# Optimization experiments

Hardware: AMD Instinct MI355X
Metric: run time of the kernel (lower is better)

Reference implementation:

```python
import jax, jax.numpy as jnp
import numpy as np

EPS = 1e-6       # eps from __init__
STEPSIZE = 1.0   # stepsize from __init__
DELTA = 0.1      # delta from __init__


def setup_inputs() -> dict:
    key = jax.random.key(0)
    k1, k2, k3 = jax.random.split(key, 3)
    N, L, H, E, M = 2, 2048, 8, 64, 64
    return {
        "queries": jax.random.normal(k1, (N, L, H, E), dtype=jnp.float32),
        "keys": jax.random.normal(k2, (N, L, H, E), dtype=jnp.float32),
        "values": jax.random.normal(k3, (N, L, H, M), dtype=jnp.float32),
        "key_lengths_mask": jnp.ones((N, L), dtype=jnp.float32),
    }


def reference(queries, keys, values, key_lengths_mask):
    # elu feature map: elu(x) + 1
    Q = jax.nn.elu(queries) + 1.0                                   # [N,L,H,E]
    K = (jax.nn.elu(keys) + 1.0) * key_lengths_mask[:, :, None, None]
    N, L, H, E = Q.shape

    # normalizer Z_t = 1 / (q_t . sum_{s<=t} k_s + eps)
    Z = 1.0 / (jnp.einsum('nlhe,nlhe->nlh', Q, jnp.cumsum(K, axis=1)) + EPS)

    # per-step outer products k_s v_s^T  (original materializes this einsum)
    KV = jnp.einsum('nlhe,nlhm->nlhem', K, values)                  # [N,L,H,E,M]

    # causal_dot_product: out_t = q_t . cumsum_s(KV)_t
    out = jnp.einsum('nlhe,nlhem->nlhm', Q, jnp.cumsum(KV, axis=1)) * Z[..., None]

    # momentum coefficients mu_j from Frobenius norms over (E,M)
    diff_norm = jnp.sqrt(jnp.sum((KV[:, 1:] - KV[:, :-1]) ** 2, axis=(3, 4)))  # [N,L-1,H]
    base_norm = jnp.sqrt(jnp.sum(KV[:, :-1] ** 2, axis=(3, 4)))
    mu = jnp.clip((1.0 - jnp.sqrt(diff_norm / base_norm)) ** 2, 0.0, 1.0 - DELTA)

    # momentum weights: a_{L-1}=1, a_j = 1 + mu_j * a_{j+1} (backward recurrence).
    # This equals both momentum_weight (cumprod-sum form) and momentum_weight_old
    # (explicit reverse loop) in the original, so Kn == Kw.
    def step(a, mu_t):
        a_new = 1.0 + mu_t * a
        return a_new, a_new

    _, a_seq = jax.lax.scan(step, jnp.ones((N, H), Q.dtype),
                            jnp.moveaxis(mu, 1, 0), reverse=True)   # [L-1,N,H]
    momentum_weight = jnp.concatenate(
        [jnp.moveaxis(a_seq, 0, 1), jnp.ones((N, 1, H), Q.dtype)], axis=1)  # [N,L,H]
    Kn = K * momentum_weight[..., None] * STEPSIZE                  # [N,L,H,E]

    return out, Kn
```

## Files before the change

kernel.cpp:

```cpp
#include <hip/hip_runtime.h>

#define N_ 2
#define L_ 2048
#define H_ 8
#define NH_ 16
#define NC_ 32
#define EPS_ 1e-6f
#define DELTA_ 0.1f

#define CHSZ 4160
#define ST_SHORTS (NH_*NC_*CHSZ)
#define KV_SHORTS (NH_*L_*64)

typedef short s8v __attribute__((ext_vector_type(8)));
typedef short s4v __attribute__((ext_vector_type(4)));
typedef float f4v __attribute__((ext_vector_type(4)));

__device__ __forceinline__ float elup1(float x){ return x>0.f ? x+1.f : __expf(x); }
__device__ __forceinline__ short f2b(float x){
  unsigned u = __float_as_uint(x);
  return (short)((u + 0x7FFFu + ((u>>16)&1u)) >> 16);
}
__device__ __forceinline__ float b2f(short s){
  return __uint_as_float(((unsigned)(unsigned short)s) << 16);
}

__global__ __launch_bounds__(256) void kA(const float* __restrict__ keys,
    const float* __restrict__ values, const float* __restrict__ mask,
    unsigned short* __restrict__ st, short* __restrict__ ktil,
    short* __restrict__ vtilT, float* __restrict__ mu)
{
  const int bid = blockIdx.x, c = bid & (NC_-1), nh = bid >> 5;
  const int n = nh >> 3, h = nh & 7, tid = threadIdx.x;
  const int lane = tid & 63, w = tid >> 6, r = lane & 15, g = lane >> 4;

  __shared__ __attribute__((aligned(16))) short Ktb[64][72];
  __shared__ __attribute__((aligned(16))) short Vtb[80][72];
  __shared__ float prt[6][4][64];

  #pragma unroll
  for (int i = 0; i < 4; ++i) {
    const int idx4 = tid + 256*i;
    const int t = idx4 >> 4, e4 = (idx4 & 15) << 2;
    const int l = c*64 + t;
    const size_t b = (((size_t)n*L_ + l)*H_ + h)*64 + e4;
    const float m0 = mask[n*L_ + l];
    const f4v kx = *(const f4v*)&keys[b];
    const f4v vx = *(const f4v*)&values[b];
    s4v kb4;
    #pragma unroll
    for (int j = 0; j < 4; ++j) kb4[j] = f2b(elup1(kx[j]) * m0);
    *(s4v*)&ktil[((size_t)nh*L_ + l)*64 + e4] = kb4;
    #pragma unroll
    for (int j = 0; j < 4; ++j) { Ktb[e4+j][t] = kb4[j]; Vtb[e4+j][t] = f2b(vx[j]); }
  }
  if (tid < 64) Vtb[64][tid] = (short)0x3F80;
  __syncthreads();

  #pragma unroll
  for (int i = 0; i < 2; ++i) {
    const int idx8 = tid + 256*i;
    const int m = idx8 >> 3, t8 = (idx8 & 7) << 3;
    *(s8v*)&vtilT[((size_t)bid*64 + m)*64 + t8] = *(const s8v*)&Vtb[m][t8];
  }

  {
    f4v acc[5];
    #pragma unroll
    for (int j = 0; j < 5; ++j) acc[j] = (f4v)(0.f);
    #pragma unroll
    for (int k2 = 0; k2 < 2; ++k2) {
      const s8v a = *(const s8v*)&Ktb[w*16 + r][k2*32 + g*8];
      #pragma unroll
      for (int mj = 0; mj < 5; ++mj) {
        const s8v bb = *(const s8v*)&Vtb[mj*16 + r][k2*32 + g*8];
        acc[mj] = __builtin_amdgcn_mfma_f32_16x16x32_bf16(a, bb, acc[mj], 0, 0, 0);
      }
    }
    unsigned short* sp = st + (size_t)bid*CHSZ;
    #pragma unroll
    for (int mj = 0; mj < 5; ++mj) {
      const int m = mj*16 + r;
      if (m <= 64) {
        s4v pk;
        #pragma unroll
        for (int j = 0; j < 4; ++j) pk[j] = f2b(acc[mj][j]);
        *(s4v*)&sp[(size_t)m*64 + w*16 + g*4] = pk;
      }
    }
  }

  {
    const int t = lane, eq = w;
    const int l = c*64 + t;
    const int l1 = (l+1 < L_) ? l+1 : l;
    const size_t b0 = (((size_t)n*L_ + l )*H_ + h)*64 + eq*16;
    const size_t b1 = (((size_t)n*L_ + l1)*H_ + h)*64 + eq*16;
    const float m0 = mask[n*L_ + l], m1 = mask[n*L_ + l1];
    float kk0=0.f,kk1=0.f,knn=0.f,vv0=0.f,vv1=0.f,vnn=0.f;
    #pragma unroll
    for (int j = 0; j < 16; j += 4) {
      const f4v ka = *(const f4v*)&keys[b0+j];
      const f4v kc = *(const f4v*)&keys[b1+j];
      const f4v va = *(const f4v*)&values[b0+j];
      const f4v vc = *(const f4v*)&values[b1+j];
      #pragma unroll
      for (int jj = 0; jj < 4; ++jj) {
        const float k0 = elup1(ka[jj])*m0, k1 = elup1(kc[jj])*m1;
        kk0 += k0*k0; kk1 += k1*k1; knn += k0*k1;
        const float v0 = va[jj], v1 = vc[jj];
        vv0 += v0*v0; vv1 += v1*v1; vnn += v0*v1;
      }
    }
    prt[0][eq][t]=kk0; prt[1][eq][t]=kk1; prt[2][eq][t]=knn;
    prt[3][eq][t]=vv0; prt[4][eq][t]=vv1; prt[5][eq][t]=vnn;
  }
  __syncthreads();
  if (tid < 64) {
    float s[6];
    #pragma unroll
    for (int q2 = 0; q2 < 6; ++q2)
      s[q2] = prt[q2][0][tid]+prt[q2][1][tid]+prt[q2][2][tid]+prt[q2][3][tid];
    const int j = c*64 + tid;
    float mval = 0.f;
    if (j < L_-1) {
      const float base2 = s[0]*s[3];
      float diff2 = s[1]*s[4] - 2.f*s[2]*s[5] + base2;
      diff2 = fmaxf(diff2, 0.f);
      if (base2 > 0.f) {
        const float r4 = sqrtf(sqrtf(diff2/base2));
        const float om = 1.f - r4;
        mval = fminf(om*om, 1.f - DELTA_);
      } else {
        mval = 1.f - DELTA_;
      }
    }
    mu[(size_t)nh*L_ + j] = mval;
  }
}

__global__ __launch_bounds__(256) void kBC(unsigned short* __restrict__ st,
    const float* __restrict__ mu, float* __restrict__ aw)
{
  const int bx = blockIdx.x, tid = threadIdx.x;
  if (bx < 260) {
    const int id = bx*256 + tid;
    const int nh2 = id / CHSZ;
    const int elem = id - nh2*CHSZ;
    unsigned short* base = st + (size_t)nh2*NC_*CHSZ + elem;
    unsigned short rr[NC_];
    #pragma unroll
    for (int c2 = 0; c2 < NC_; ++c2) rr[c2] = base[(size_t)c2*CHSZ];
    float acc = 0.f;
    #pragma unroll
    for (int c2 = 0; c2 < NC_; ++c2) {
      const float v = b2f((short)rr[c2]);
      base[(size_t)c2*CHSZ] = (unsigned short)f2b(acc);
      acc += v;
    }
    return;
  }
  const int nh2 = bx - 260;
  const float* mup = mu + (size_t)nh2*L_;
  float* awp = aw + (size_t)nh2*L_;
  __shared__ float Psc[256], Qsc[256];
  float lm[8];
  #pragma unroll
  for (int i = 0; i < 8; ++i) lm[i] = mup[tid*8 + i];
  float p = 1.f, q = 0.f;
  #pragma unroll
  for (int i = 7; i >= 0; --i) { q = lm[i]*q + 1.f; p *= lm[i]; }
  Psc[tid] = p; Qsc[tid] = q;
  __syncthreads();
  for (int d = 1; d < 256; d <<= 1) {
    float pr = 1.f, qr = 0.f;
    const bool has = (tid + d) < 256;
    if (has) { pr = Psc[tid+d]; qr = Qsc[tid+d]; }
    __syncthreads();
    if (has) { const float np = p*pr, nq = p*qr + q; p = np; q = nq; Psc[tid] = p; Qsc[tid] = q; }
    __syncthreads();
  }
  float x = (tid == 255) ? 1.f : Psc[tid+1] + Qsc[tid+1];
  #pragma unroll
  for (int i = 7; i >= 0; --i) { x = lm[i]*x + 1.f; awp[tid*8+i] = x; }
}

__global__ __launch_bounds__(256) void kD(const float* __restrict__ queries,
    const unsigned short* __restrict__ st, const short* __restrict__ ktil,
    const short* __restrict__ vtilT, const float* __restrict__ aw,
    float* __restrict__ out, float* __restrict__ kn)
{
  const int bid = blockIdx.x, c = bid & (NC_-1), nh = bid >> 5;
  const int n = nh >> 3, h = nh & 7, tid = threadIdx.x;
  const int lane = tid & 63, w = tid >> 6, r = lane & 15, g = lane >> 4;

  __shared__ __attribute__((aligned(16))) short Qb[64][72];
  __shared__ __attribute__((aligned(16))) short Kb[64][72];
  __shared__ __attribute__((aligned(16))) short Vtb[80][72];
  __shared__ __attribute__((aligned(16))) union {
    struct { short Pb[64][72]; short Sb[80][72]; } d;
    float outf[64][68];
  } U;
  __shared__ float Zl[64], al[64];

  #pragma unroll
  for (int i = 0; i < 4; ++i) {
    const int idx4 = tid + 256*i;
    const int t = idx4 >> 4, e4 = (idx4 & 15) << 2;
    const int l = c*64 + t;
    const f4v qx = *(const f4v*)&queries[(((size_t)n*L_ + l)*H_ + h)*64 + e4];
    s4v qb4;
    #pragma unroll
    for (int j = 0; j < 4; ++j) qb4[j] = f2b(elup1(qx[j]));
    *(s4v*)&Qb[t][e4] = qb4;
  }
  for (int idx = tid; idx < 512; idx += 256) {
    const int t = idx >> 3, e8 = (idx & 7) << 3;
    *(s8v*)&Kb[t][e8] = *(const s8v*)&ktil[((size_t)nh*L_ + c*64 + t)*64 + e8];
  }
  #pragma unroll
  for (int i = 0; i < 2; ++i) {
    const int idx8 = tid + 256*i;
    const int m = idx8 >> 3, t8 = (idx8 & 7) << 3;
    *(s8v*)&Vtb[m][t8] = *(const s8v*)&vtilT[((size_t)bid*64 + m)*64 + t8];
  }
  for (int idx = tid; idx < 16*72; idx += 256) {
    const int rr = idx/72, cc = idx - rr*72;
    Vtb[64+rr][cc] = (rr==0 && cc<64) ? (short)0x3F80 : (short)0;
  }
  {
    const unsigned short* sp = st + (size_t)bid*CHSZ;
    for (int idx = tid; idx < 520; idx += 256) {
      const int m = idx >> 3, e8 = (idx & 7) << 3;
      *(s8v*)&U.d.Sb[m][e8] = *(const s8v*)&sp[(size_t)m*64 + e8];
    }
    for (int idx = 520 + tid; idx < 640; idx += 256) {
      *(s8v*)&U.d.Sb[idx>>3][(idx&7)<<3] = (s8v)(0);
    }
  }
  if (tid < 64) al[tid] = aw[(size_t)nh*L_ + c*64 + tid];
  __syncthreads();

  {
    f4v pacc[4];
    #pragma unroll
    for (int tj = 0; tj < 4; ++tj) pacc[tj] = (f4v)(0.f);
    #pragma unroll
    for (int k2 = 0; k2 < 2; ++k2) {
      const s8v a = *(const s8v*)&Kb[w*16 + r][k2*32 + g*8];
      #pragma unroll
      for (int tj = 0; tj < 4; ++tj) {
        const s8v bb = *(const s8v*)&Qb[tj*16 + r][k2*32 + g*8];
        pacc[tj] = __builtin_amdgcn_mfma_f32_16x16x32_bf16(a, bb, pacc[tj], 0, 0, 0);
      }
    }
    #pragma unroll
    for (int tj = 0; tj < 4; ++tj) {
      const int t = tj*16 + r;
      s4v pk;
      #pragma unroll
      for (int j = 0; j < 4; ++j) {
        const int s2 = w*16 + g*4 + j;
        pk[j] = (s2 <= t) ? f2b(pacc[tj][j]) : (short)0;
      }
      *(s4v*)&U.d.Pb[t][w*16 + g*4] = pk;
    }
  }
  __syncthreads();

  f4v oacc[5];
  #pragma unroll
  for (int j = 0; j < 5; ++j) oacc[j] = (f4v)(0.f);
  #pragma unroll
  for (int k2 = 0; k2 < 4; ++k2) {
    const s8v a = (k2 < 2) ? *(const s8v*)&Qb[w*16 + r][k2*32 + g*8]
                           : *(const s8v*)&U.d.Pb[w*16 + r][(k2-2)*32 + g*8];
    #pragma unroll
    for (int mj = 0; mj < 5; ++mj) {
      const s8v bb = (k2 < 2) ? *(const s8v*)&U.d.Sb[mj*16 + r][k2*32 + g*8]
                              : *(const s8v*)&Vtb[mj*16 + r][(k2-2)*32 + g*8];
      oacc[mj] = __builtin_amdgcn_mfma_f32_16x16x32_bf16(a, bb, oacc[mj], 0, 0, 0);
    }
  }
  __syncthreads();

  if (r == 0) {
    #pragma unroll
    for (int j = 0; j < 4; ++j) Zl[w*16 + g*4 + j] = 1.f / (oacc[4][j] + EPS_);
  }
  #pragma unroll
  for (int mj = 0; mj < 4; ++mj)
    #pragma unroll
    for (int j = 0; j < 4; ++j)
      U.outf[w*16 + g*4 + j][mj*16 + r] = oacc[mj][j];
  __syncthreads();

  for (int idx = tid; idx < 1024; idx += 256) {
    const int t = idx >> 4, m4 = (idx & 15) << 2, l = c*64 + t;
    f4v v = *(const f4v*)&U.outf[t][m4];
    const float z = Zl[t];
    v[0] *= z; v[1] *= z; v[2] *= z; v[3] *= z;
    __builtin_nontemporal_store(v, (f4v*)&out[(((size_t)n*L_ + l)*H_ + h)*64 + m4]);
  }
  for (int idx = tid; idx < 1024; idx += 256) {
    const int t = idx >> 4, e4 = (idx & 15) << 2, l = c*64 + t;
    const float a2 = al[t];
    const s4v kb4 = *(const s4v*)&Kb[t][e4];
    f4v o;
    #pragma unroll
    for (int j = 0; j < 4; ++j) o[j] = b2f(kb4[j]) * a2;
    __builtin_nontemporal_store(o, (f4v*)&kn[(((size_t)n*L_ + l)*H_ + h)*64 + e4]);
  }
}

extern "C" void kernel_launch(void* const* d_in, const int* in_sizes, int n_in,
                              void* d_out, int out_size, void* d_ws, size_t ws_size,
                              hipStream_t stream) {
  (void)in_sizes; (void)n_in; (void)out_size; (void)ws_size;
  const float* queries = (const float*)d_in[0];
  const float* keys    = (const float*)d_in[1];
  const float* values  = (const float*)d_in[2];
  const float* mask    = (const float*)d_in[3];
  float* out = (float*)d_out;
  float* kn  = out + (size_t)N_*L_*H_*64;

  unsigned short* st = (unsigned short*)d_ws;
  short* ktil = (short*)(st + ST_SHORTS);
  short* vtilT = ktil + KV_SHORTS;
  float* mu = (float*)(vtilT + KV_SHORTS);
  float* aw = mu + NH_*L_;

  hipLaunchKernelGGL(kA,  dim3(NH_*NC_), dim3(256), 0, stream,
                     keys, values, mask, st, ktil, vtilT, mu);
  hipLaunchKernelGGL(kBC, dim3(276),     dim3(256), 0, stream, st, mu, aw);
  hipLaunchKernelGGL(kD,  dim3(NH_*NC_), dim3(256), 0, stream,
                     queries, st, ktil, vtilT, aw, out, kn);
}
```

Before: 28.62 us.

## Halve chunk length to 32 and remap MFMA warp work for more blocks

Chunk length drops from 64 to 32 and the chunk count rises to 64 per (n,h), doubling the grid of the chunk-state and output kernels. Warp work in kD is redistributed: each warp computes one 16x16 tile of the causal score block and a three-column slice of the output/normalizer MFMAs. The norm-reduction pass is reorganised to 8 slices of 32 timesteps. The aim is better CU occupancy from more, smaller blocks. The cost is twice as many chunk states written to and read from global memory, plus a longer cross-chunk scan in the middle kernel.

```diff
diff --git a/kernel.cpp b/kernel.cpp
--- a/kernel.cpp
+++ b/kernel.cpp
@@ -4,7 +4,8 @@
 #define L_ 2048
 #define H_ 8
 #define NH_ 16
-#define NC_ 32
+#define C_ 32
+#define NC_ 64
 #define EPS_ 1e-6f
 #define DELTA_ 0.1f
 
@@ -30,19 +31,19 @@
     unsigned short* __restrict__ st, short* __restrict__ ktil,
     short* __restrict__ vtilT, float* __restrict__ mu)
 {
-  const int bid = blockIdx.x, c = bid & (NC_-1), nh = bid >> 5;
+  const int bid = blockIdx.x, c = bid & (NC_-1), nh = bid >> 6;
   const int n = nh >> 3, h = nh & 7, tid = threadIdx.x;
   const int lane = tid & 63, w = tid >> 6, r = lane & 15, g = lane >> 4;
 
-  __shared__ __attribute__((aligned(16))) short Ktb[64][72];
-  __shared__ __attribute__((aligned(16))) short Vtb[80][72];
-  __shared__ float prt[6][4][64];
-
-  #pragma unroll
-  for (int i = 0; i < 4; ++i) {
+  __shared__ __attribute__((aligned(16))) short Ktb[64][40];
+  __shared__ __attribute__((aligned(16))) short Vtb[80][40];
+  __shared__ float prt[6][8][32];
+
+  #pragma unroll
+  for (int i = 0; i < 2; ++i) {
     const int idx4 = tid + 256*i;
     const int t = idx4 >> 4, e4 = (idx4 & 15) << 2;
-    const int l = c*64 + t;
+    const int l = c*C_ + t;
     const size_t b = (((size_t)n*L_ + l)*H_ + h)*64 + e4;
     const float m0 = mask[n*L_ + l];
     const f4v kx = *(const f4v*)&keys[b];
@@ -54,28 +55,26 @@
     #pragma unroll
     for (int j = 0; j < 4; ++j) { Ktb[e4+j][t] = kb4[j]; Vtb[e4+j][t] = f2b(vx[j]); }
   }
-  if (tid < 64) Vtb[64][tid] = (short)0x3F80;
-  __syncthreads();
-
-  #pragma unroll
-  for (int i = 0; i < 2; ++i) {
-    const int idx8 = tid + 256*i;
-    const int m = idx8 >> 3, t8 = (idx8 & 7) << 3;
-    *(s8v*)&vtilT[((size_t)bid*64 + m)*64 + t8] = *(const s8v*)&Vtb[m][t8];
+  for (int idx = tid; idx < 16*40; idx += 256) {
+    const int rr2 = idx/40, cc2 = idx - rr2*40;
+    Vtb[64+rr2][cc2] = (rr2==0 && cc2<C_) ? (short)0x3F80 : (short)0;
+  }
+  __syncthreads();
+
+  {
+    const int m = tid >> 2, t8 = (tid & 3) << 3;
+    *(s8v*)&vtilT[((size_t)bid*64 + m)*C_ + t8] = *(const s8v*)&Vtb[m][t8];
   }
 
   {
     f4v acc[5];
     #pragma unroll
     for (int j = 0; j < 5; ++j) acc[j] = (f4v)(0.f);
-    #pragma unroll
-    for (int k2 = 0; k2 < 2; ++k2) {
-      const s8v a = *(const s8v*)&Ktb[w*16 + r][k2*32 + g*8];
-      #pragma unroll
-      for (int mj = 0; mj < 5; ++mj) {
-        const s8v bb = *(const s8v*)&Vtb[mj*16 + r][k2*32 + g*8];
-        acc[mj] = __builtin_amdgcn_mfma_f32_16x16x32_bf16(a, bb, acc[mj], 0, 0, 0);
-      }
+    const s8v a = *(const s8v*)&Ktb[w*16 + r][g*8];
+    #pragma unroll
+    for (int mj = 0; mj < 5; ++mj) {
+      const s8v bb = *(const s8v*)&Vtb[mj*16 + r][g*8];
+      acc[mj] = __builtin_amdgcn_mfma_f32_16x16x32_bf16(a, bb, acc[mj], 0, 0, 0);
     }
     unsigned short* sp = st + (size_t)bid*CHSZ;
     #pragma unroll
@@ -91,15 +90,15 @@
   }
 
   {
-    const int t = lane, eq = w;
-    const int l = c*64 + t;
+    const int t = tid & 31, eq = tid >> 5;
+    const int l = c*C_ + t;
     const int l1 = (l+1 < L_) ? l+1 : l;
-    const size_t b0 = (((size_t)n*L_ + l )*H_ + h)*64 + eq*16;
-    const size_t b1 = (((size_t)n*L_ + l1)*H_ + h)*64 + eq*16;
+    const size_t b0 = (((size_t)n*L_ + l )*H_ + h)*64 + eq*8;
+    const size_t b1 = (((size_t)n*L_ + l1)*H_ + h)*64 + eq*8;
     const float m0 = mask[n*L_ + l], m1 = mask[n*L_ + l1];
     float kk0=0.f,kk1=0.f,knn=0.f,vv0=0.f,vv1=0.f,vnn=0.f;
     #pragma unroll
-    for (int j = 0; j < 16; j += 4) {
+    for (int j = 0; j < 8; j += 4) {
       const f4v ka = *(const f4v*)&keys[b0+j];
       const f4v kc = *(const f4v*)&keys[b1+j];
       const f4v va = *(const f4v*)&values[b0+j];
@@ -116,12 +115,16 @@
     prt[3][eq][t]=vv0; prt[4][eq][t]=vv1; prt[5][eq][t]=vnn;
   }
   __syncthreads();
-  if (tid < 64) {
+  if (tid < 32) {
     float s[6];
     #pragma unroll
-    for (int q2 = 0; q2 < 6; ++q2)
-      s[q2] = prt[q2][0][tid]+prt[q2][1][tid]+prt[q2][2][tid]+prt[q2][3][tid];
-    const int j = c*64 + tid;
+    for (int q2 = 0; q2 < 6; ++q2) {
+      float acc2 = 0.f;
+      #pragma unroll
+      for (int eq = 0; eq < 8; ++eq) acc2 += prt[q2][eq][tid];
+      s[q2] = acc2;
+    }
+    const int j = c*C_ + tid;
     float mval = 0.f;
     if (j < L_-1) {
       const float base2 = s[0]*s[3];
@@ -190,43 +193,41 @@
     const short* __restrict__ vtilT, const float* __restrict__ aw,
     float* __restrict__ out, float* __restrict__ kn)
 {
-  const int bid = blockIdx.x, c = bid & (NC_-1), nh = bid >> 5;
+  const int bid = blockIdx.x, c = bid & (NC_-1), nh = bid >> 6;
   const int n = nh >> 3, h = nh & 7, tid = threadIdx.x;
   const int lane = tid & 63, w = tid >> 6, r = lane & 15, g = lane >> 4;
 
-  __shared__ __attribute__((aligned(16))) short Qb[64][72];
-  __shared__ __attribute__((aligned(16))) short Kb[64][72];
-  __shared__ __attribute__((aligned(16))) short Vtb[80][72];
+  __shared__ __attribute__((aligned(16))) short Qb[32][72];
+  __shared__ __attribute__((aligned(16))) short Kb[32][72];
+  __shared__ __attribute__((aligned(16))) short Vtb[80][40];
   __shared__ __attribute__((aligned(16))) union {
-    struct { short Pb[64][72]; short Sb[80][72]; } d;
-    float outf[64][68];
+    struct { short Pb[32][40]; short Sb[80][72]; } d;
+    float outf[32][68];
   } U;
-  __shared__ float Zl[64], al[64];
-
-  #pragma unroll
-  for (int i = 0; i < 4; ++i) {
+  __shared__ float Zl[32], al[32];
+
+  #pragma unroll
+  for (int i = 0; i < 2; ++i) {
     const int idx4 = tid + 256*i;
     const int t = idx4 >> 4, e4 = (idx4 & 15) << 2;
-    const int l = c*64 + t;
+    const int l = c*C_ + t;
     const f4v qx = *(const f4v*)&queries[(((size_t)n*L_ + l)*H_ + h)*64 + e4];
     s4v qb4;
     #pragma unroll
     for (int j = 0; j < 4; ++j) qb4[j] = f2b(elup1(qx[j]));
     *(s4v*)&Qb[t][e4] = qb4;
   }
-  for (int idx = tid; idx < 512; idx += 256) {
-    const int t = idx >> 3, e8 = (idx & 7) << 3;
-    *(s8v*)&Kb[t][e8] = *(const s8v*)&ktil[((size_t)nh*L_ + c*64 + t)*64 + e8];
-  }
-  #pragma unroll
-  for (int i = 0; i < 2; ++i) {
-    const int idx8 = tid + 256*i;
-    const int m = idx8 >> 3, t8 = (idx8 & 7) << 3;
-    *(s8v*)&Vtb[m][t8] = *(const s8v*)&vtilT[((size_t)bid*64 + m)*64 + t8];
-  }
-  for (int idx = tid; idx < 16*72; idx += 256) {
-    const int rr = idx/72, cc = idx - rr*72;
-    Vtb[64+rr][cc] = (rr==0 && cc<64) ? (short)0x3F80 : (short)0;
+  {
+    const int t = tid >> 3, e8 = (tid & 7) << 3;
+    *(s8v*)&Kb[t][e8] = *(const s8v*)&ktil[((size_t)nh*L_ + c*C_ + t)*64 + e8];
+  }
+  {
+    const int m = tid >> 2, t8 = (tid & 3) << 3;
+    *(s8v*)&Vtb[m][t8] = *(const s8v*)&vtilT[((size_t)bid*64 + m)*C_ + t8];
+  }
+  for (int idx = tid; idx < 16*40; idx += 256) {
+    const int rr2 = idx/40, cc2 = idx - rr2*40;
+    Vtb[64+rr2][cc2] = (rr2==0 && cc2<C_) ? (short)0x3F80 : (short)0;
   }
   {
     const unsigned short* sp = st + (size_t)bid*CHSZ;
@@ -238,72 +239,78 @@
       *(s8v*)&U.d.Sb[idx>>3][(idx&7)<<3] = (s8v)(0);
     }
   }
-  if (tid < 64) al[tid] = aw[(size_t)nh*L_ + c*64 + tid];
-  __syncthreads();
-
-  {
-    f4v pacc[4];
-    #pragma unroll
-    for (int tj = 0; tj < 4; ++tj) pacc[tj] = (f4v)(0.f);
+  if (tid < 32) al[tid] = aw[(size_t)nh*L_ + c*C_ + tid];
+  __syncthreads();
+
+  {
+    const int st2 = w >> 1, tt2 = w & 1;
+    f4v pacc = (f4v)(0.f);
     #pragma unroll
     for (int k2 = 0; k2 < 2; ++k2) {
-      const s8v a = *(const s8v*)&Kb[w*16 + r][k2*32 + g*8];
+      const s8v a = *(const s8v*)&Kb[st2*16 + r][k2*32 + g*8];
+      const s8v bb = *(const s8v*)&Qb[tt2*16 + r][k2*32 + g*8];
+      pacc = __builtin_amdgcn_mfma_f32_16x16x32_bf16(a, bb, pacc, 0, 0, 0);
+    }
+    const int t = tt2*16 + r;
+    s4v pk;
+    #pragma unroll
+    for (int j = 0; j < 4; ++j) {
+      const int s2 = st2*16 + g*4 + j;
+      pk[j] = (s2 <= t) ? f2b(pacc[j]) : (short)0;
+    }
+    *(s4v*)&U.d.Pb[t][st2*16 + g*4] = pk;
+  }
+  __syncthreads();
+
+  const int wt = w & 1;
+  const int mbase = (w >> 1) * 3;
+  f4v oacc[3];
+  #pragma unroll
+  for (int j = 0; j < 3; ++j) oacc[j] = (f4v)(0.f);
+  #pragma unroll
+  for (int k2 = 0; k2 < 3; ++k2) {
+    const s8v a = (k2 < 2) ? *(const s8v*)&Qb[wt*16 + r][k2*32 + g*8]
+                           : *(const s8v*)&U.d.Pb[wt*16 + r][g*8];
+    #pragma unroll
+    for (int mi = 0; mi < 3; ++mi) {
+      const int mj = mbase + mi;
+      if (mj < 5) {
+        const s8v bb = (k2 < 2) ? *(const s8v*)&U.d.Sb[mj*16 + r][k2*32 + g*8]
+                                : *(const s8v*)&Vtb[mj*16 + r][g*8];
+        oacc[mi] = __builtin_amdgcn_mfma_f32_16x16x32_bf16(a, bb, oacc[mi], 0, 0, 0);
+      }
+    }
+  }
+  __syncthreads();
+
+  if (mbase == 3 && r == 0) {
+    #pragma unroll
+    for (int j = 0; j < 4; ++j) Zl[wt*16 + g*4 + j] = 1.f / (oacc[1][j] + EPS_);
+  }
+  #pragma unroll
+  for (int mi = 0; mi < 3; ++mi) {
+    const int mj = mbase + mi;
+    if (mj < 4) {
       #pragma unroll
-      for (int tj = 0; tj < 4; ++tj) {
-        const s8v bb = *(const s8v*)&Qb[tj*16 + r][k2*32 + g*8];
-        pacc[tj] = __builtin_amdgcn_mfma_f32_16x16x32_bf16(a, bb, pacc[tj], 0, 0, 0);
-      }
-    }
-    #pragma unroll
-    for (int tj = 0; tj < 4; ++tj) {
-      const int t = tj*16 + r;
-      s4v pk;
-      #pragma unroll
-      for (int j = 0; j < 4; ++j) {
-        const int s2 = w*16 + g*4 + j;
-        pk[j] = (s2 <= t) ? f2b(pacc[tj][j]) : (short)0;
-      }
-      *(s4v*)&U.d.Pb[t][w*16 + g*4] = pk;
-    }
-  }
-  __syncthreads();
-
-  f4v oacc[5];
-  #pragma unroll
-  for (int j = 0; j < 5; ++j) oacc[j] = (f4v)(0.f);
-  #pragma unroll
-  for (int k2 = 0; k2 < 4; ++k2) {
-    const s8v a = (k2 < 2) ? *(const s8v*)&Qb[w*16 + r][k2*32 + g*8]
-                           : *(const s8v*)&U.d.Pb[w*16 + r][(k2-2)*32 + g*8];
-    #pragma unroll
-    for (int mj = 0; mj < 5; ++mj) {
-      const s8v bb = (k2 < 2) ? *(const s8v*)&U.d.Sb[mj*16 + r][k2*32 + g*8]
-                              : *(const s8v*)&Vtb[mj*16 + r][(k2-2)*32 + g*8];
-      oacc[mj] = __builtin_amdgcn_mfma_f32_16x16x32_bf16(a, bb, oacc[mj], 0, 0, 0);
-    }
-  }
-  __syncthreads();
-
-  if (r == 0) {
-    #pragma unroll
-    for (int j = 0; j < 4; ++j) Zl[w*16 + g*4 + j] = 1.f / (oacc[4][j] + EPS_);
-  }
-  #pragma unroll
-  for (int mj = 0; mj < 4; ++mj)
-    #pragma unroll
-    for (int j = 0; j < 4; ++j)
-      U.outf[w*16 + g*4 + j][mj*16 + r] = oacc[mj][j];
-  __syncthreads();
-
-  for (int idx = tid; idx < 1024; idx += 256) {
-    const int t = idx >> 4, m4 = (idx & 15) << 2, l = c*64 + t;
+      for (int j = 0; j < 4; ++j)
+        U.outf[wt*16 + g*4 + j][mj*16 + r] = oacc[mi][j];
+    }
+  }
+  __syncthreads();
+
+  #pragma unroll
+  for (int i = 0; i < 2; ++i) {
+    const int idx4 = tid + 256*i;
+    const int t = idx4 >> 4, m4 = (idx4 & 15) << 2, l = c*C_ + t;
     f4v v = *(const f4v*)&U.outf[t][m4];
     const float z = Zl[t];
     v[0] *= z; v[1] *= z; v[2] *= z; v[3] *= z;
     __builtin_nontemporal_store(v, (f4v*)&out[(((size_t)n*L_ + l)*H_ + h)*64 + m4]);
   }
-  for (int idx = tid; idx < 1024; idx += 256) {
-    const int t = idx >> 4, e4 = (idx & 15) << 2, l = c*64 + t;
+  #pragma unroll
+  for (int i = 0; i < 2; ++i) {
+    const int idx4 = tid + 256*i;
+    const int t = idx4 >> 4, e4 = (idx4 & 15) << 2, l = c*C_ + t;
     const float a2 = al[t];
     const s4v kb4 = *(const s4v*)&Kb[t][e4];
     f4v o;
```

New measurement: 30.00 us. 1.05x slower.

## Load state and V fragments straight into registers and store output from accumulators

Applied to the files above, without the earlier changes.

In kD, the per-chunk state matrix and transposed V tile are now read from global memory directly into MFMA B-operand registers instead of being staged through shared memory. The normalizer is broadcast with a warp shuffle, and outputs are written straight from the accumulators without the shared-memory transpose. This cuts LDS footprint, two barriers, and the LDS copy traffic. The price is higher register pressure and scalar 4-byte output stores, which coalesce less well than the earlier 16-byte vector stores.

```diff
diff --git a/kernel.cpp b/kernel.cpp
--- a/kernel.cpp
+++ b/kernel.cpp
@@ -4,6 +4,7 @@
 #define L_ 2048
 #define H_ 8
 #define NH_ 16
+#define C_ 64
 #define NC_ 32
 #define EPS_ 1e-6f
 #define DELTA_ 0.1f
@@ -42,7 +43,7 @@
   for (int i = 0; i < 4; ++i) {
     const int idx4 = tid + 256*i;
     const int t = idx4 >> 4, e4 = (idx4 & 15) << 2;
-    const int l = c*64 + t;
+    const int l = c*C_ + t;
     const size_t b = (((size_t)n*L_ + l)*H_ + h)*64 + e4;
     const float m0 = mask[n*L_ + l];
     const f4v kx = *(const f4v*)&keys[b];
@@ -92,7 +93,7 @@
 
   {
     const int t = lane, eq = w;
-    const int l = c*64 + t;
+    const int l = c*C_ + t;
     const int l1 = (l+1 < L_) ? l+1 : l;
     const size_t b0 = (((size_t)n*L_ + l )*H_ + h)*64 + eq*16;
     const size_t b1 = (((size_t)n*L_ + l1)*H_ + h)*64 + eq*16;
@@ -121,7 +122,7 @@
     #pragma unroll
     for (int q2 = 0; q2 < 6; ++q2)
       s[q2] = prt[q2][0][tid]+prt[q2][1][tid]+prt[q2][2][tid]+prt[q2][3][tid];
-    const int j = c*64 + tid;
+    const int j = c*C_ + tid;
     float mval = 0.f;
     if (j < L_-1) {
       const float base2 = s[0]*s[3];
@@ -196,19 +197,29 @@
 
   __shared__ __attribute__((aligned(16))) short Qb[64][72];
   __shared__ __attribute__((aligned(16))) short Kb[64][72];
-  __shared__ __attribute__((aligned(16))) short Vtb[80][72];
-  __shared__ __attribute__((aligned(16))) union {
-    struct { short Pb[64][72]; short Sb[80][72]; } d;
-    float outf[64][68];
-  } U;
-  __shared__ float Zl[64], al[64];
+  __shared__ __attribute__((aligned(16))) short Pb[64][72];
+  __shared__ float al[64];
+
+  const unsigned short* sp = st + (size_t)bid*CHSZ;
+  const short* vp = vtilT + (size_t)bid*64*64;
+
+  s8v sfrag[2][4], srow64[2];
+  const s8v zero8 = (s8v)(0);
+  #pragma unroll
+  for (int k2 = 0; k2 < 2; ++k2) {
+    #pragma unroll
+    for (int mj = 0; mj < 4; ++mj)
+      sfrag[k2][mj] = *(const s8v*)&sp[(size_t)(mj*16 + r)*64 + k2*32 + g*8];
+    srow64[k2] = (r == 0) ? *(const s8v*)&sp[(size_t)64*64 + k2*32 + g*8] : zero8;
+  }
 
   #pragma unroll
   for (int i = 0; i < 4; ++i) {
     const int idx4 = tid + 256*i;
     const int t = idx4 >> 4, e4 = (idx4 & 15) << 2;
-    const int l = c*64 + t;
-    const f4v qx = *(const f4v*)&queries[(((size_t)n*L_ + l)*H_ + h)*64 + e4];
+    const int l = c*C_ + t;
+    const f4v qx = __builtin_nontemporal_load(
+        (const f4v*)&queries[(((size_t)n*L_ + l)*H_ + h)*64 + e4]);
     s4v qb4;
     #pragma unroll
     for (int j = 0; j < 4; ++j) qb4[j] = f2b(elup1(qx[j]));
@@ -216,29 +227,9 @@
   }
   for (int idx = tid; idx < 512; idx += 256) {
     const int t = idx >> 3, e8 = (idx & 7) << 3;
-    *(s8v*)&Kb[t][e8] = *(const s8v*)&ktil[((size_t)nh*L_ + c*64 + t)*64 + e8];
-  }
-  #pragma unroll
-  for (int i = 0; i < 2; ++i) {
-    const int idx8 = tid + 256*i;
-    const int m = idx8 >> 3, t8 = (idx8 & 7) << 3;
-    *(s8v*)&Vtb[m][t8] = *(const s8v*)&vtilT[((size_t)bid*64 + m)*64 + t8];
-  }
-  for (int idx = tid; idx < 16*72; idx += 256) {
-    const int rr = idx/72, cc = idx - rr*72;
-    Vtb[64+rr][cc] = (rr==0 && cc<64) ? (short)0x3F80 : (short)0;
-  }
-  {
-    const unsigned short* sp = st + (size_t)bid*CHSZ;
-    for (int idx = tid; idx < 520; idx += 256) {
-      const int m = idx >> 3, e8 = (idx & 7) << 3;
-      *(s8v*)&U.d.Sb[m][e8] = *(const s8v*)&sp[(size_t)m*64 + e8];
-    }
-    for (int idx = 520 + tid; idx < 640; idx += 256) {
-      *(s8v*)&U.d.Sb[idx>>3][(idx&7)<<3] = (s8v)(0);
-    }
-  }
-  if (tid < 64) al[tid] = aw[(size_t)nh*L_ + c*64 + tid];
+    *(s8v*)&Kb[t][e8] = *(const s8v*)&ktil[((size_t)nh*L_ + c*C_ + t)*64 + e8];
+  }
+  if (tid < 64) al[tid] = aw[(size_t)nh*L_ + c*C_ + tid];
   __syncthreads();
 
   {
@@ -263,8 +254,21 @@
         const int s2 = w*16 + g*4 + j;
         pk[j] = (s2 <= t) ? f2b(pacc[tj][j]) : (short)0;
       }
-      *(s4v*)&U.d.Pb[t][w*16 + g*4] = pk;
-    }
+      *(s4v*)&Pb[t][w*16 + g*4] = pk;
+    }
+  }
+
+  s8v vfrag[2][4], vones;
+  #pragma unroll
+  for (int k2 = 0; k2 < 2; ++k2)
+    #pragma unroll
+    for (int mj = 0; mj < 4; ++mj)
+      vfrag[k2][mj] = *(const s8v*)&vp[(size_t)(mj*16 + r)*64 + k2*32 + g*8];
+  {
+    s8v o;
+    #pragma unroll
+    for (int j = 0; j < 8; ++j) o[j] = (short)0x3F80;
+    vones = (r == 0) ? o : zero8;
   }
   __syncthreads();
 
@@ -274,36 +278,34 @@
   #pragma unroll
   for (int k2 = 0; k2 < 4; ++k2) {
     const s8v a = (k2 < 2) ? *(const s8v*)&Qb[w*16 + r][k2*32 + g*8]
-                           : *(const s8v*)&U.d.Pb[w*16 + r][(k2-2)*32 + g*8];
+                           : *(const s8v*)&Pb[w*16 + r][(k2-2)*32 + g*8];
     #pragma unroll
     for (int mj = 0; mj < 5; ++mj) {
-      const s8v bb = (k2 < 2) ? *(const s8v*)&U.d.Sb[mj*16 + r][k2*32 + g*8]
-                              : *(const s8v*)&Vtb[mj*16 + r][(k2-2)*32 + g*8];
+      const s8v bb = (k2 < 2) ? ((mj < 4) ? sfrag[k2][mj] : srow64[k2])
+                              : ((mj < 4) ? vfrag[k2-2][mj] : vones);
       oacc[mj] = __builtin_amdgcn_mfma_f32_16x16x32_bf16(a, bb, oacc[mj], 0, 0, 0);
     }
   }
-  __syncthreads();
-
-  if (r == 0) {
-    #pragma unroll
-    for (int j = 0; j < 4; ++j) Zl[w*16 + g*4 + j] = 1.f / (oacc[4][j] + EPS_);
-  }
-  #pragma unroll
-  for (int mj = 0; mj < 4; ++mj)
-    #pragma unroll
-    for (int j = 0; j < 4; ++j)
-      U.outf[w*16 + g*4 + j][mj*16 + r] = oacc[mj][j];
-  __syncthreads();
-
-  for (int idx = tid; idx < 1024; idx += 256) {
-    const int t = idx >> 4, m4 = (idx & 15) << 2, l = c*64 + t;
-    f4v v = *(const f4v*)&U.outf[t][m4];
-    const float z = Zl[t];
-    v[0] *= z; v[1] *= z; v[2] *= z; v[3] *= z;
-    __builtin_nontemporal_store(v, (f4v*)&out[(((size_t)n*L_ + l)*H_ + h)*64 + m4]);
-  }
-  for (int idx = tid; idx < 1024; idx += 256) {
-    const int t = idx >> 4, e4 = (idx & 15) << 2, l = c*64 + t;
+
+  {
+    float z[4];
+    #pragma unroll
+    for (int j = 0; j < 4; ++j) {
+      const float dj = __shfl(oacc[4][j], g << 4);
+      z[j] = 1.f / (dj + EPS_);
+    }
+    float* obase = out + (((size_t)n*L_ + c*C_ + w*16)*H_ + h)*64;
+    #pragma unroll
+    for (int mj = 0; mj < 4; ++mj)
+      #pragma unroll
+      for (int j = 0; j < 4; ++j)
+        __builtin_nontemporal_store(oacc[mj][j] * z[j],
+            &obase[(size_t)(g*4 + j)*H_*64 + mj*16 + r]);
+  }
+  #pragma unroll
+  for (int i = 0; i < 4; ++i) {
+    const int idx4 = tid + 256*i;
+    const int t = idx4 >> 4, e4 = (idx4 & 15) << 2, l = c*C_ + t;
     const float a2 = al[t];
     const s4v kb4 = *(const s4v*)&Kb[t][e4];
     f4v o;
```

Result: slower. 29.45 us (+2.9%).
